# Optimization experiments

Measured on AMD Instinct MI355X. Metric: run time of the kernel, lower is better.

The kernel has to match this reference:

```python
import jax, jax.numpy as jnp
import numpy as np

BATCH, E = 4096, 8
DIMS = [512, 1024, 1024, 512]


def setup_inputs() -> dict:
    key = jax.random.key(0)
    ks = jax.random.split(key, 8)
    inp = {
        'weight_blend': jax.random.uniform(ks[0], (BATCH, E), dtype=jnp.float32),
        'x': jax.random.normal(ks[1], (BATCH, DIMS[0]), dtype=jnp.float32),
    }
    for i in range(3):
        inp[f'W{i}'] = jax.random.normal(ks[2 + i], (E, DIMS[i + 1], DIMS[i]), dtype=jnp.float32)
        inp[f'B{i}'] = jnp.zeros((E, DIMS[i + 1]), dtype=jnp.float32)
    return inp


def _blended_layer(weight_blend, x, W, B):
    # Fused form of: weight = sum_e blend[b,e]*W[e]; y = bmm(weight, x) + sum_e blend[b,e]*B[e]
    # Computed as sum_e blend_e * (W_e @ x) without materializing (batch,out,in).
    y = jnp.einsum('eoi,bi->beo', W, x)          # per-expert GEMM, (B,E,out)
    y = jnp.einsum('be,beo->bo', weight_blend, y)  # blend combine
    return y + weight_blend @ B                   # blended bias (B,out)


def reference(weight_blend, x, W0, B0, W1, B1, W2, B2):
    # Dropout with keep_prob=0.0 is identity in eval mode; activations: elu, elu, linear.
    h = jax.nn.elu(_blended_layer(weight_blend, x, W0, B0))
    h = jax.nn.elu(_blended_layer(weight_blend, h, W1, B1))
    out = _blended_layer(weight_blend, h, W2, B2)
    return out
```

## Files before the change

kernel.cpp:

```cpp
#include <hip/hip_runtime.h>
#include <cstdint>
#include <cstddef>

typedef __bf16 bf16x8 __attribute__((ext_vector_type(8)));
typedef float f32x4 __attribute__((ext_vector_type(4)));
typedef unsigned short u16;
typedef unsigned short u16x8 __attribute__((ext_vector_type(8)));

#define BATCH 4096
#define NE 8

__device__ __forceinline__ u16 f2bf(float f) {
  union { float f; uint32_t u; } v; v.f = f;
  uint32_t u = v.u;
  u += 0x7fffu + ((u >> 16) & 1u);
  return (u16)(u >> 16);
}

__device__ __forceinline__ float bf2f(u16 u) {
  union { uint32_t u; float f; } v; v.u = ((uint32_t)u) << 16;
  return v.f;
}

__device__ __forceinline__ void cast8(const float* src, u16* dst) {
  const float4* p = (const float4*)src;
  float4 a = p[0], b = p[1];
  u16x8 o;
  o[0] = f2bf(a.x); o[1] = f2bf(a.y); o[2] = f2bf(a.z); o[3] = f2bf(a.w);
  o[4] = f2bf(b.x); o[5] = f2bf(b.y); o[6] = f2bf(b.z); o[7] = f2bf(b.w);
  *(u16x8*)dst = o;
}

__device__ __forceinline__ void conv_w_chunk(const float* __restrict__ W,
                                             u16* __restrict__ Bt,
                                             int N, int K0, int chunk) {
  int per_row = K0 >> 3;
  int rid = chunk / per_row;
  int i0 = (chunk - rid * per_row) << 3;
  int e = rid / N;
  int o = rid - e * N;
  cast8(W + (size_t)rid * K0 + i0,
        Bt + (size_t)o * ((size_t)NE * K0) + (size_t)e * K0 + i0);
}

__global__ void prep_kernel(const float* __restrict__ x,
                            const float* __restrict__ W0,
                            const float* __restrict__ W1,
                            const float* __restrict__ W2,
                            u16* __restrict__ h0, u16* __restrict__ Bt0,
                            u16* __restrict__ Bt1, u16* __restrict__ Bt2) {
  int t = blockIdx.x * blockDim.x + threadIdx.x;
  const int C0 = BATCH * 512 / 8;
  const int C1 = C0 + NE * 1024 * 512 / 8;
  const int C2 = C1 + NE * 1024 * 1024 / 8;
  if (t < C0) {
    cast8(x + (size_t)t * 8, h0 + (size_t)t * 8);
  } else if (t < C1) {
    conv_w_chunk(W0, Bt0, 1024, 512, t - C0);
  } else if (t < C2) {
    conv_w_chunk(W1, Bt1, 1024, 1024, t - C1);
  } else {
    conv_w_chunk(W2, Bt2, 512, 1024, t - C2);
  }
}

template<bool ELU_ACT, bool OUT_BF16>
__global__ void combine8_kernel(const u16* __restrict__ P,
                                const float* __restrict__ blend,
                                const float* __restrict__ Bias,
                                void* __restrict__ outp, int N) {
  int t = blockIdx.x * blockDim.x + threadIdx.x;
  int per_row = N >> 3;
  int b = t / per_row;
  int i0 = (t - b * per_row) << 3;
  const size_t slice = (size_t)BATCH * N;
  const float4* blp = (const float4*)(blend + b * NE);
  float4 u0 = blp[0], u1 = blp[1];
  float bl[8] = {u0.x, u0.y, u0.z, u0.w, u1.x, u1.y, u1.z, u1.w};
  float v[8] = {0, 0, 0, 0, 0, 0, 0, 0};
  #pragma unroll
  for (int e = 0; e < NE; ++e) {
    u16x8 pv = *(const u16x8*)(P + (size_t)e * slice + (size_t)b * N + i0);
    #pragma unroll
    for (int j = 0; j < 8; ++j) v[j] += bl[e] * bf2f(pv[j]);
  }
  #pragma unroll
  for (int e = 0; e < NE; ++e) {
    const float4* bp = (const float4*)(Bias + (size_t)e * N + i0);
    float4 ba = bp[0], bb = bp[1];
    float bv[8] = {ba.x, ba.y, ba.z, ba.w, bb.x, bb.y, bb.z, bb.w};
    #pragma unroll
    for (int j = 0; j < 8; ++j) v[j] += bl[e] * bv[j];
  }
  if (ELU_ACT) {
    #pragma unroll
    for (int j = 0; j < 8; ++j) v[j] = v[j] > 0.f ? v[j] : expm1f(v[j]);
  }
  if (OUT_BF16) {
    u16x8 o;
    #pragma unroll
    for (int j = 0; j < 8; ++j) o[j] = f2bf(v[j]);
    *(u16x8*)((u16*)outp + (size_t)b * N + i0) = o;
  } else {
    float4* op = (float4*)((float*)outp + (size_t)b * N + i0);
    op[0] = (float4){v[0], v[1], v[2], v[3]};
    op[1] = (float4){v[4], v[5], v[6], v[7]};
  }
}

#define GL2LDS(g, l) __builtin_amdgcn_global_load_lds( \
    (__attribute__((address_space(1))) void*)(g),      \
    (__attribute__((address_space(3))) void*)(l), 16, 0, 0)

template<int K0, int NB>
__global__ __launch_bounds__(256, 4)
void gemm_be_kernel(const u16* __restrict__ h, const u16* __restrict__ Bt,
                    u16* __restrict__ P, int N) {
  __shared__ __align__(16) u16 Hs[128 * 64];
  __shared__ __align__(16) u16 Bs[128 * 64];

  const int tid  = threadIdx.x;
  const int w    = tid >> 6, lane = tid & 63;
  const int wm   = w >> 1,   wn   = w & 1;
  const int lrow = lane & 15, quad = lane >> 4;

  const int bid    = blockIdx.x;
  const int combos = NB * NE;
  const int combo  = bid % combos;
  const int rowb   = bid / combos;
  const int e      = combo & 7;
  const int colb   = combo >> 3;
  const int row0 = rowb * 128;
  const int col0 = colb * 128;
  const int EK   = K0 * NE;

  const int trow = tid >> 3;
  const int tcol = (tid & 7) ^ (trow & 7);
  const u16* gH = h + (size_t)(row0 + trow) * K0 + (tcol << 3);
  const u16* gB = Bt + (size_t)(col0 + trow) * EK + (size_t)e * K0 + (tcol << 3);
  u16* lH = &Hs[tid * 8];
  u16* lB = &Bs[tid * 8];

  const int xr = lrow & 7;
  const u16* fH[2][4];
  const u16* fB[2][4];
  #pragma unroll
  for (int kc = 0; kc < 2; ++kc)
    #pragma unroll
    for (int i = 0; i < 4; ++i) {
      fH[kc][i] = &Hs[(wm * 64 + i * 16 + lrow) * 64 + (((kc * 4 + quad) ^ xr) << 3)];
      fB[kc][i] = &Bs[(wn * 64 + i * 16 + lrow) * 64 + (((kc * 4 + quad) ^ xr) << 3)];
    }

  f32x4 acc[4][4];
  #pragma unroll
  for (int i = 0; i < 4; ++i)
    #pragma unroll
    for (int j = 0; j < 4; ++j) acc[i][j] = (f32x4){0.f, 0.f, 0.f, 0.f};

  for (int it = 0; it < K0 / 64; ++it) {
    #pragma unroll
    for (int i = 0; i < 4; ++i) {
      GL2LDS(gH + (size_t)(32 * i) * K0, lH + 2048 * i);
      GL2LDS(gB + (size_t)(32 * i) * EK, lB + 2048 * i);
    }
    gH += 64; gB += 64;
    __syncthreads();

    #pragma unroll
    for (int kc = 0; kc < 2; ++kc) {
      bf16x8 hf[4], bfr[4];
      #pragma unroll
      for (int i = 0; i < 4; ++i) hf[i] = *(const bf16x8*)fH[kc][i];
      #pragma unroll
      for (int j = 0; j < 4; ++j) bfr[j] = *(const bf16x8*)fB[kc][j];
      #pragma unroll
      for (int i = 0; i < 4; ++i)
        #pragma unroll
        for (int j = 0; j < 4; ++j)
          acc[i][j] = __builtin_amdgcn_mfma_f32_16x16x32_bf16(hf[i], bfr[j], acc[i][j], 0, 0, 0);
    }
    __syncthreads();
  }

  u16* Ps = P + (size_t)e * ((size_t)BATCH * N);
  u16* ls = &Hs[w * 2048];
  #pragma unroll
  for (int half = 0; half < 2; ++half) {
    #pragma unroll
    for (int mh = 0; mh < 2; ++mh) {
      int mt = half * 2 + mh;
      #pragma unroll
      for (int r = 0; r < 4; ++r) {
        int rloc = mh * 16 + quad * 4 + r;
        #pragma unroll
        for (int nt = 0; nt < 4; ++nt) {
          int col = nt * 16 + lrow;
          int c8 = (col >> 3) ^ (rloc & 7);
          ls[rloc * 64 + (c8 << 3) + (col & 7)] = f2bf(acc[mt][nt][r]);
        }
      }
    }
    #pragma unroll
    for (int p = 0; p < 4; ++p) {
      int rloc = p * 8 + (lane >> 3);
      int c8 = (lane & 7) ^ (rloc & 7);
      u16x8 v = *(const u16x8*)&ls[rloc * 64 + (c8 << 3)];
      int row = row0 + wm * 64 + half * 32 + rloc;
      int colg = col0 + wn * 64 + ((lane & 7) << 3);
      *(u16x8*)&Ps[(size_t)row * N + colg] = v;
    }
  }
}

extern "C" void kernel_launch(void* const* d_in, const int* in_sizes, int n_in,
                              void* d_out, int out_size, void* d_ws, size_t ws_size,
                              hipStream_t stream) {
  const float* blend = (const float*)d_in[0];
  const float* x  = (const float*)d_in[1];
  const float* W0 = (const float*)d_in[2];
  const float* B0 = (const float*)d_in[3];
  const float* W1 = (const float*)d_in[4];
  const float* B1 = (const float*)d_in[5];
  const float* W2 = (const float*)d_in[6];
  const float* B2 = (const float*)d_in[7];
  float* out = (float*)d_out;

  char* ws = (char*)d_ws;
  u16* hA  = (u16*)ws;
  u16* h1  = (u16*)(ws + 8388608);
  u16* Bt0 = (u16*)(ws + 16777216);
  u16* Bt1 = (u16*)(ws + 25165824);
  u16* Bt2 = (u16*)(ws + 41943040);
  u16* P   = (u16*)(ws + 50331648);

  prep_kernel<<<9216, 256, 0, stream>>>(x, W0, W1, W2, hA, Bt0, Bt1, Bt2);

  gemm_be_kernel<512, 8><<<2048, 256, 0, stream>>>(hA, Bt0, P, 1024);
  combine8_kernel<true, true><<<2048, 256, 0, stream>>>(P, blend, B0, h1, 1024);

  gemm_be_kernel<1024, 8><<<2048, 256, 0, stream>>>(h1, Bt1, P, 1024);
  combine8_kernel<true, true><<<2048, 256, 0, stream>>>(P, blend, B1, hA, 1024);

  gemm_be_kernel<1024, 4><<<1024, 256, 0, stream>>>(hA, Bt2, P, 512);
  combine8_kernel<false, false><<<1024, 256, 0, stream>>>(P, blend, B2, out, 512);
}
```

Measured before the change: 347.9 us.

## Fold blend weighting into GEMM epilogue, reducing per-expert partial slices

Each GEMM block now loops over several experts, scales each expert's accumulator by the per-row blend weight held in LDS, and writes one partial sum per expert group instead of one per expert. The combine kernel then only sums 2 or 4 bf16 slices instead of weighting 8. This cuts the partial-result traffic written and read through global memory. In exchange, grids are much smaller (512 blocks), occupancy drops with launch bounds of 2 and a second accumulator set, and the H tile is reloaded once per expert.

```diff
diff --git a/kernel.cpp b/kernel.cpp
--- a/kernel.cpp
+++ b/kernel.cpp
@@ -64,8 +64,8 @@
   }
 }
 
-template<bool ELU_ACT, bool OUT_BF16>
-__global__ void combine8_kernel(const u16* __restrict__ P,
+template<int SLICES, bool ELU_ACT, bool OUT_BF16>
+__global__ void combineS_kernel(const u16* __restrict__ P,
                                 const float* __restrict__ blend,
                                 const float* __restrict__ Bias,
                                 void* __restrict__ outp, int N) {
@@ -74,16 +74,16 @@
   int b = t / per_row;
   int i0 = (t - b * per_row) << 3;
   const size_t slice = (size_t)BATCH * N;
+  float v[8] = {0, 0, 0, 0, 0, 0, 0, 0};
+  #pragma unroll
+  for (int s = 0; s < SLICES; ++s) {
+    u16x8 pv = *(const u16x8*)(P + (size_t)s * slice + (size_t)b * N + i0);
+    #pragma unroll
+    for (int j = 0; j < 8; ++j) v[j] += bf2f(pv[j]);
+  }
   const float4* blp = (const float4*)(blend + b * NE);
   float4 u0 = blp[0], u1 = blp[1];
   float bl[8] = {u0.x, u0.y, u0.z, u0.w, u1.x, u1.y, u1.z, u1.w};
-  float v[8] = {0, 0, 0, 0, 0, 0, 0, 0};
-  #pragma unroll
-  for (int e = 0; e < NE; ++e) {
-    u16x8 pv = *(const u16x8*)(P + (size_t)e * slice + (size_t)b * N + i0);
-    #pragma unroll
-    for (int j = 0; j < 8; ++j) v[j] += bl[e] * bf2f(pv[j]);
-  }
   #pragma unroll
   for (int e = 0; e < NE; ++e) {
     const float4* bp = (const float4*)(Bias + (size_t)e * N + i0);
@@ -112,32 +112,38 @@
     (__attribute__((address_space(1))) void*)(g),      \
     (__attribute__((address_space(3))) void*)(l), 16, 0, 0)
 
-template<int K0, int NB>
-__global__ __launch_bounds__(256, 4)
-void gemm_be_kernel(const u16* __restrict__ h, const u16* __restrict__ Bt,
-                    u16* __restrict__ P, int N) {
+template<int K0, int EPB>
+__global__ __launch_bounds__(256, 2)
+void gemm_fold_kernel(const u16* __restrict__ h, const u16* __restrict__ Bt,
+                      const float* __restrict__ blend,
+                      u16* __restrict__ P, int N) {
   __shared__ __align__(16) u16 Hs[128 * 64];
   __shared__ __align__(16) u16 Bs[128 * 64];
+  __shared__ float bls[128 * 9];
 
   const int tid  = threadIdx.x;
   const int w    = tid >> 6, lane = tid & 63;
   const int wm   = w >> 1,   wn   = w & 1;
   const int lrow = lane & 15, quad = lane >> 4;
 
-  const int bid    = blockIdx.x;
-  const int combos = NB * NE;
-  const int combo  = bid % combos;
-  const int rowb   = bid / combos;
-  const int e      = combo & 7;
-  const int colb   = combo >> 3;
-  const int row0 = rowb * 128;
-  const int col0 = colb * 128;
+  const int row0 = blockIdx.x * 128;
+  const int col0 = blockIdx.y * 128;
+  const int e0   = blockIdx.z * EPB;
   const int EK   = K0 * NE;
+
+  {
+    const float4 bv = ((const float4*)(blend + (size_t)row0 * NE))[tid];
+    int row = tid >> 1, c0 = (tid & 1) * 4;
+    bls[row * 9 + c0 + 0] = bv.x;
+    bls[row * 9 + c0 + 1] = bv.y;
+    bls[row * 9 + c0 + 2] = bv.z;
+    bls[row * 9 + c0 + 3] = bv.w;
+  }
 
   const int trow = tid >> 3;
   const int tcol = (tid & 7) ^ (trow & 7);
   const u16* gH = h + (size_t)(row0 + trow) * K0 + (tcol << 3);
-  const u16* gB = Bt + (size_t)(col0 + trow) * EK + (size_t)e * K0 + (tcol << 3);
+  const u16* gB = Bt + (size_t)(col0 + trow) * EK + (size_t)e0 * K0 + (tcol << 3);
   u16* lH = &Hs[tid * 8];
   u16* lB = &Bs[tid * 8];
 
@@ -158,32 +164,57 @@
     #pragma unroll
     for (int j = 0; j < 4; ++j) acc[i][j] = (f32x4){0.f, 0.f, 0.f, 0.f};
 
-  for (int it = 0; it < K0 / 64; ++it) {
-    #pragma unroll
-    for (int i = 0; i < 4; ++i) {
-      GL2LDS(gH + (size_t)(32 * i) * K0, lH + 2048 * i);
-      GL2LDS(gB + (size_t)(32 * i) * EK, lB + 2048 * i);
-    }
-    gH += 64; gB += 64;
-    __syncthreads();
-
-    #pragma unroll
-    for (int kc = 0; kc < 2; ++kc) {
-      bf16x8 hf[4], bfr[4];
-      #pragma unroll
-      for (int i = 0; i < 4; ++i) hf[i] = *(const bf16x8*)fH[kc][i];
-      #pragma unroll
-      for (int j = 0; j < 4; ++j) bfr[j] = *(const bf16x8*)fB[kc][j];
-      #pragma unroll
-      for (int i = 0; i < 4; ++i)
-        #pragma unroll
-        for (int j = 0; j < 4; ++j)
-          acc[i][j] = __builtin_amdgcn_mfma_f32_16x16x32_bf16(hf[i], bfr[j], acc[i][j], 0, 0, 0);
-    }
-    __syncthreads();
-  }
-
-  u16* Ps = P + (size_t)e * ((size_t)BATCH * N);
+  #pragma unroll 1
+  for (int ee = 0; ee < EPB; ++ee) {
+    f32x4 acc2[4][4];
+    #pragma unroll
+    for (int i = 0; i < 4; ++i)
+      #pragma unroll
+      for (int j = 0; j < 4; ++j) acc2[i][j] = (f32x4){0.f, 0.f, 0.f, 0.f};
+
+    const u16* pH = gH;
+    const u16* pB = gB + (size_t)ee * K0;
+
+    for (int it = 0; it < K0 / 64; ++it) {
+      #pragma unroll
+      for (int i = 0; i < 4; ++i) {
+        GL2LDS(pH + (size_t)(32 * i) * K0, lH + 2048 * i);
+        GL2LDS(pB + (size_t)(32 * i) * EK, lB + 2048 * i);
+      }
+      pH += 64; pB += 64;
+      __syncthreads();
+
+      #pragma unroll
+      for (int kc = 0; kc < 2; ++kc) {
+        bf16x8 hf[4], bfr[4];
+        #pragma unroll
+        for (int i = 0; i < 4; ++i) hf[i] = *(const bf16x8*)fH[kc][i];
+        #pragma unroll
+        for (int j = 0; j < 4; ++j) bfr[j] = *(const bf16x8*)fB[kc][j];
+        #pragma unroll
+        for (int i = 0; i < 4; ++i)
+          #pragma unroll
+          for (int j = 0; j < 4; ++j)
+            acc2[i][j] = __builtin_amdgcn_mfma_f32_16x16x32_bf16(hf[i], bfr[j], acc2[i][j], 0, 0, 0);
+      }
+      __syncthreads();
+    }
+
+    #pragma unroll
+    for (int mt = 0; mt < 4; ++mt) {
+      float bl[4];
+      #pragma unroll
+      for (int r = 0; r < 4; ++r)
+        bl[r] = bls[(wm * 64 + mt * 16 + quad * 4 + r) * 9 + (e0 + ee)];
+      #pragma unroll
+      for (int nt = 0; nt < 4; ++nt)
+        #pragma unroll
+        for (int r = 0; r < 4; ++r)
+          acc[mt][nt][r] += bl[r] * acc2[mt][nt][r];
+    }
+  }
+
+  u16* Ps = P + (size_t)blockIdx.z * ((size_t)BATCH * N);
   u16* ls = &Hs[w * 2048];
   #pragma unroll
   for (int half = 0; half < 2; ++half) {
@@ -236,12 +267,12 @@
 
   prep_kernel<<<9216, 256, 0, stream>>>(x, W0, W1, W2, hA, Bt0, Bt1, Bt2);
 
-  gemm_be_kernel<512, 8><<<2048, 256, 0, stream>>>(hA, Bt0, P, 1024);
-  combine8_kernel<true, true><<<2048, 256, 0, stream>>>(P, blend, B0, h1, 1024);
-
-  gemm_be_kernel<1024, 8><<<2048, 256, 0, stream>>>(h1, Bt1, P, 1024);
-  combine8_kernel<true, true><<<2048, 256, 0, stream>>>(P, blend, B1, hA, 1024);
-
-  gemm_be_kernel<1024, 4><<<1024, 256, 0, stream>>>(hA, Bt2, P, 512);
-  combine8_kernel<false, false><<<1024, 256, 0, stream>>>(P, blend, B2, out, 512);
-}
+  gemm_fold_kernel<512, 4><<<dim3(32, 8, 2), 256, 0, stream>>>(hA, Bt0, blend, P, 1024);
+  combineS_kernel<2, true, true><<<2048, 256, 0, stream>>>(P, blend, B0, h1, 1024);
+
+  gemm_fold_kernel<1024, 4><<<dim3(32, 8, 2), 256, 0, stream>>>(h1, Bt1, blend, P, 1024);
+  combineS_kernel<2, true, true><<<2048, 256, 0, stream>>>(P, blend, B1, hA, 1024);
+
+  gemm_fold_kernel<1024, 2><<<dim3(32, 4, 4), 256, 0, stream>>>(hA, Bt2, blend, P, 512);
+  combineS_kernel<4, false, false><<<1024, 256, 0, stream>>>(P, blend, B2, out, 512);
+}
```

Result: faster. 287.5 us (-17.4%).
